# Kernel tuning notes

Measured on AMD Instinct MI355X. Metric: run time of the kernel, lower is better.

The kernel has to match this reference:

```python
import jax, jax.numpy as jnp
import numpy as np

B, S, RNN, ATT_HID = 64, 2048, 1024, 512


def setup_inputs() -> dict:
    key = jax.random.key(0)
    ks = jax.random.split(key, 8)
    h = jax.random.normal(ks[0], (B, RNN), dtype=jnp.float32)
    att_feats = jax.random.normal(ks[1], (B, S, RNN), dtype=jnp.float32)
    p_att_feats = jax.random.normal(ks[2], (B, S, ATT_HID), dtype=jnp.float32)
    att_masks = jax.random.randint(ks[3], (B, S), 0, 2, dtype=jnp.int32)
    # parameters of h2att: Linear(rnn_size -> att_hid_size)
    W_h = jax.random.normal(ks[4], (ATT_HID, RNN), dtype=jnp.float32) / np.sqrt(RNN)
    b_h = jnp.zeros((ATT_HID,), dtype=jnp.float32)
    # parameters of alpha_net: Linear(att_hid_size -> 1)
    w_a = jax.random.normal(ks[5], (ATT_HID,), dtype=jnp.float32) / np.sqrt(ATT_HID)
    b_a = jnp.zeros((), dtype=jnp.float32)
    return {"h": h, "att_feats": att_feats, "p_att_feats": p_att_feats,
            "att_masks": att_masks, "W_h": W_h, "b_h": b_h, "w_a": w_a, "b_a": b_a}


def reference(h, att_feats, p_att_feats, att_masks, W_h, b_h, w_a, b_a):
    # h: [B, rnn], p_att_feats: [B, S, att_hid], att_feats: [B, S, feat]
    att_h = h @ W_h.T + b_h                            # [B, att_hid]
    dot = jnp.tanh(p_att_feats + att_h[:, None, :])     # [B, S, att_hid]
    scores = jnp.einsum('bsh,h->bs', dot, w_a) + b_a    # [B, S]
    weight = jax.nn.softmax(scores, axis=1)             # [B, S]
    m = att_masks.astype(weight.dtype)
    weight = weight * m
    weight = weight / jnp.sum(weight, axis=1, keepdims=True)
    att_res = jnp.einsum('bs,bsd->bd', weight, att_feats)  # [B, feat]
    return att_res
```

## Files before the change

kernel.cpp:

```cpp
#include <hip/hip_runtime.h>

#define B_SZ 64
#define S_SZ 2048
#define RNN 1024
#define ATT 512
#define NCHUNK 32
#define CHUNK_S (S_SZ / NCHUNK)
#define KSPL 2

#define OFF_ATTHP  0
#define OFF_PART   65536
#define OFF_USUM   2162688

__device__ __forceinline__ float fast_tanh(float x) {
    float t = __builtin_exp2f(x * 2.885390082f);
    return 1.0f - 2.0f * __builtin_amdgcn_rcpf(t + 1.0f);
}

__global__ __launch_bounds__(128) void k_atth(const float* __restrict__ h,
                                              const float* __restrict__ Wh,
                                              float* __restrict__ att_h_part) {
    int b  = blockIdx.z;
    int ks = blockIdx.y;
    int j  = blockIdx.x * 128 + threadIdx.x;
    int kbase = ks * (RNN / KSPL);

    __shared__ float hs[RNN / KSPL];
    for (int i = threadIdx.x; i < RNN / KSPL; i += 128)
        hs[i] = h[(size_t)b * RNN + kbase + i];
    __syncthreads();

    const float4* w4 = (const float4*)(Wh + (size_t)j * RNN + kbase);
    const float4* h4 = (const float4*)hs;
    float a0 = 0.f, a1 = 0.f, a2 = 0.f, a3 = 0.f;
    #pragma unroll 4
    for (int k = 0; k < (RNN / KSPL) / 4; k += 4) {
        float4 w, hv;
        w = w4[k + 0]; hv = h4[k + 0];
        a0 += w.x * hv.x + w.y * hv.y + w.z * hv.z + w.w * hv.w;
        w = w4[k + 1]; hv = h4[k + 1];
        a1 += w.x * hv.x + w.y * hv.y + w.z * hv.z + w.w * hv.w;
        w = w4[k + 2]; hv = h4[k + 2];
        a2 += w.x * hv.x + w.y * hv.y + w.z * hv.z + w.w * hv.w;
        w = w4[k + 3]; hv = h4[k + 3];
        a3 += w.x * hv.x + w.y * hv.y + w.z * hv.z + w.w * hv.w;
    }
    att_h_part[((size_t)ks * B_SZ + b) * ATT + j] = (a0 + a1) + (a2 + a3);
}

__global__ __launch_bounds__(256) void k_fused(const float* __restrict__ p,
                                               const float* __restrict__ att_h_part,
                                               const float* __restrict__ bh,
                                               const float* __restrict__ w_a,
                                               const float* __restrict__ b_a,
                                               const int* __restrict__ mask,
                                               const float* __restrict__ feats,
                                               float* __restrict__ partials,
                                               float* __restrict__ usum) {
    int c = blockIdx.x;
    int b = blockIdx.y;
    int t = threadIdx.x;
    int s0 = c * CHUNK_S;

    __shared__ float ah[ATT];
    __shared__ float wa[ATT];
    __shared__ float u_c[CHUNK_S];
    __shared__ int   active[CHUNK_S];
    __shared__ int   nact_s;

    const float* ph0 = att_h_part + (size_t)b * ATT;
    const float* ph1 = att_h_part + ((size_t)B_SZ + b) * ATT;
    for (int i = t; i < ATT; i += 256) {
        ah[i] = ph0[i] + ph1[i] + bh[i];
        wa[i] = w_a[i];
    }
    if (t < CHUNK_S) {
        u_c[t] = 0.f;
        int m = mask[(size_t)b * S_SZ + s0 + t];
        unsigned long long bal = __ballot(m != 0);
        int rank = __popcll(bal & ((1ULL << (unsigned)t) - 1ULL));
        if (m) active[rank] = t;
        if (t == 0) nact_s = (int)__popcll(bal);
    }
    __syncthreads();
    int nact = nact_s;

    int wave = t >> 6;
    int lane = t & 63;
    float ba = b_a[0];

    const float4* ah4 = (const float4*)ah;
    const float4* wa4 = (const float4*)wa;
    float4 a0 = ah4[lane];
    float4 a1 = ah4[64 + lane];
    float4 w0 = wa4[lane];
    float4 w1 = wa4[64 + lane];

    const float4* pbase = (const float4*)(p + ((size_t)b * S_SZ + s0) * ATT);
    for (int k = wave; k < nact; k += 4) {
        int sl = active[k];
        const float4* p4 = pbase + (size_t)sl * 128;
        float4 x0 = p4[lane];
        float4 x1 = p4[64 + lane];

        float part;
        part  = w0.x * fast_tanh(x0.x + a0.x);
        part += w0.y * fast_tanh(x0.y + a0.y);
        part += w0.z * fast_tanh(x0.z + a0.z);
        part += w0.w * fast_tanh(x0.w + a0.w);
        part += w1.x * fast_tanh(x1.x + a1.x);
        part += w1.y * fast_tanh(x1.y + a1.y);
        part += w1.z * fast_tanh(x1.z + a1.z);
        part += w1.w * fast_tanh(x1.w + a1.w);

        #pragma unroll
        for (int off = 32; off > 0; off >>= 1)
            part += __shfl_xor(part, off, 64);

        if (lane == 0) {
            float sc = fminf(part + ba, 80.f);
            u_c[k] = __builtin_expf(sc);
        }
    }
    __syncthreads();

    const float4* f4 = (const float4*)(feats + ((size_t)b * S_SZ + s0) * RNN);
    float4 acc = {0.f, 0.f, 0.f, 0.f};
    int k = 0;
    for (; k + 4 <= nact; k += 4) {
        int r0 = active[k + 0], r1 = active[k + 1];
        int r2 = active[k + 2], r3 = active[k + 3];
        float g0 = u_c[k + 0], g1 = u_c[k + 1];
        float g2 = u_c[k + 2], g3 = u_c[k + 3];
        float4 v0 = f4[(size_t)r0 * 256 + t];
        float4 v1 = f4[(size_t)r1 * 256 + t];
        float4 v2 = f4[(size_t)r2 * 256 + t];
        float4 v3 = f4[(size_t)r3 * 256 + t];
        acc.x += g0 * v0.x; acc.y += g0 * v0.y; acc.z += g0 * v0.z; acc.w += g0 * v0.w;
        acc.x += g1 * v1.x; acc.y += g1 * v1.y; acc.z += g1 * v1.z; acc.w += g1 * v1.w;
        acc.x += g2 * v2.x; acc.y += g2 * v2.y; acc.z += g2 * v2.z; acc.w += g2 * v2.w;
        acc.x += g3 * v3.x; acc.y += g3 * v3.y; acc.z += g3 * v3.z; acc.w += g3 * v3.w;
    }
    for (; k < nact; ++k) {
        int r = active[k];
        float g = u_c[k];
        float4 v = f4[(size_t)r * 256 + t];
        acc.x += g * v.x; acc.y += g * v.y; acc.z += g * v.z; acc.w += g * v.w;
    }
    ((float4*)partials)[((size_t)b * NCHUNK + c) * 256 + t] = acc;

    if (wave == 0) {
        float s = u_c[lane];
        #pragma unroll
        for (int off = 32; off > 0; off >>= 1)
            s += __shfl_xor(s, off, 64);
        if (lane == 0) usum[(size_t)b * NCHUNK + c] = s;
    }
}

__global__ __launch_bounds__(256) void k_reduce(const float* __restrict__ partials,
                                                const float* __restrict__ usum,
                                                float* __restrict__ out) {
    int b = blockIdx.y;
    int j = blockIdx.x * 256 + threadIdx.x;

    float tot = 0.f;
    #pragma unroll
    for (int c = 0; c < NCHUNK; ++c)
        tot += usum[(size_t)b * NCHUNK + c];

    float acc = 0.f;
    #pragma unroll 8
    for (int c = 0; c < NCHUNK; ++c)
        acc += partials[((size_t)b * NCHUNK + c) * RNN + j];

    out[(size_t)b * RNN + j] = acc / tot;
}

extern "C" void kernel_launch(void* const* d_in, const int* in_sizes, int n_in,
                              void* d_out, int out_size, void* d_ws, size_t ws_size,
                              hipStream_t stream) {
    const float* h         = (const float*)d_in[0];
    const float* att_feats = (const float*)d_in[1];
    const float* p_att     = (const float*)d_in[2];
    const int*   att_masks = (const int*)d_in[3];
    const float* W_h       = (const float*)d_in[4];
    const float* b_h       = (const float*)d_in[5];
    const float* w_a       = (const float*)d_in[6];
    const float* b_a       = (const float*)d_in[7];
    float* out = (float*)d_out;

    float* wsf = (float*)d_ws;
    float* att_h_part = wsf + OFF_ATTHP;
    float* partials   = wsf + OFF_PART;
    float* usum       = wsf + OFF_USUM;

    k_atth<<<dim3(4, KSPL, B_SZ), 128, 0, stream>>>(h, W_h, att_h_part);
    k_fused<<<dim3(NCHUNK, B_SZ), 256, 0, stream>>>(p_att, att_h_part, b_h, w_a, b_a,
                                                    att_masks, att_feats,
                                                    partials, usum);
    k_reduce<<<dim3(RNN / 256, B_SZ), 256, 0, stream>>>(partials, usum, out);
}
```

Before: 103.7 us.

## Software-pipeline score computation with feature gather in 16-row tiles

```diff
diff --git a/kernel.cpp b/kernel.cpp
--- a/kernel.cpp
+++ b/kernel.cpp
@@ -48,15 +48,15 @@
     att_h_part[((size_t)ks * B_SZ + b) * ATT + j] = (a0 + a1) + (a2 + a3);
 }
 
-__global__ __launch_bounds__(256) void k_fused(const float* __restrict__ p,
-                                               const float* __restrict__ att_h_part,
-                                               const float* __restrict__ bh,
-                                               const float* __restrict__ w_a,
-                                               const float* __restrict__ b_a,
-                                               const int* __restrict__ mask,
-                                               const float* __restrict__ feats,
-                                               float* __restrict__ partials,
-                                               float* __restrict__ usum) {
+__global__ __launch_bounds__(256, 8) void k_fused(const float* __restrict__ p,
+                                                  const float* __restrict__ att_h_part,
+                                                  const float* __restrict__ bh,
+                                                  const float* __restrict__ w_a,
+                                                  const float* __restrict__ b_a,
+                                                  const int* __restrict__ mask,
+                                                  const float* __restrict__ feats,
+                                                  float* __restrict__ partials,
+                                                  float* __restrict__ usum) {
     int c = blockIdx.x;
     int b = blockIdx.y;
     int t = threadIdx.x;
@@ -64,8 +64,8 @@
 
     __shared__ float ah[ATT];
     __shared__ float wa[ATT];
-    __shared__ float u_c[CHUNK_S];
-    __shared__ int   active[CHUNK_S];
+    __shared__ __align__(16) float u_c[CHUNK_S];
+    __shared__ __align__(16) int   active[CHUNK_S];
     __shared__ int   nact_s;
 
     const float* ph0 = att_h_part + (size_t)b * ATT;
@@ -78,12 +78,19 @@
         u_c[t] = 0.f;
         int m = mask[(size_t)b * S_SZ + s0 + t];
         unsigned long long bal = __ballot(m != 0);
-        int rank = __popcll(bal & ((1ULL << (unsigned)t) - 1ULL));
-        if (m) active[rank] = t;
-        if (t == 0) nact_s = (int)__popcll(bal);
+        int na = (int)__popcll(bal);
+        unsigned long long below = (1ULL << (unsigned)t) - 1ULL;
+        if (m) {
+            active[__popcll(bal & below)] = t;
+        } else {
+            active[na + __popcll((~bal) & below)] = 0;
+        }
+        if (t == 0) nact_s = na;
     }
     __syncthreads();
     int nact = nact_s;
+    int n16 = (nact + 15) & ~15;
+    int n_tiles = n16 >> 4;
 
     int wave = t >> 6;
     int lane = t & 63;
@@ -97,56 +104,91 @@
     float4 w1 = wa4[64 + lane];
 
     const float4* pbase = (const float4*)(p + ((size_t)b * S_SZ + s0) * ATT);
-    for (int k = wave; k < nact; k += 4) {
-        int sl = active[k];
-        const float4* p4 = pbase + (size_t)sl * 128;
-        float4 x0 = p4[lane];
-        float4 x1 = p4[64 + lane];
-
-        float part;
-        part  = w0.x * fast_tanh(x0.x + a0.x);
-        part += w0.y * fast_tanh(x0.y + a0.y);
-        part += w0.z * fast_tanh(x0.z + a0.z);
-        part += w0.w * fast_tanh(x0.w + a0.w);
-        part += w1.x * fast_tanh(x1.x + a1.x);
-        part += w1.y * fast_tanh(x1.y + a1.y);
-        part += w1.z * fast_tanh(x1.z + a1.z);
-        part += w1.w * fast_tanh(x1.w + a1.w);
-
-        #pragma unroll
-        for (int off = 32; off > 0; off >>= 1)
-            part += __shfl_xor(part, off, 64);
-
-        if (lane == 0) {
-            float sc = fminf(part + ba, 80.f);
-            u_c[k] = __builtin_expf(sc);
+    const float4* f4 = (const float4*)(feats + ((size_t)b * S_SZ + s0) * RNN);
+    const int4*   act4 = (const int4*)active;
+    const float4* uc4  = (const float4*)u_c;
+    float4 acc = {0.f, 0.f, 0.f, 0.f};
+
+    #define SCORE_TILE(TILE)                                                    \
+    {                                                                           \
+        int base_ = ((TILE) << 4) + wave * 4;                                   \
+        _Pragma("unroll")                                                       \
+        for (int i_ = 0; i_ < 2; ++i_) {                                        \
+            int kA_ = base_ + i_ * 2, kB_ = kA_ + 1;                            \
+            int slA_ = active[kA_], slB_ = active[kB_];                         \
+            const float4* pA_ = pbase + (size_t)slA_ * 128;                     \
+            const float4* pB_ = pbase + (size_t)slB_ * 128;                     \
+            float4 xa0_ = pA_[lane];                                            \
+            float4 xa1_ = pA_[64 + lane];                                       \
+            float4 xb0_ = pB_[lane];                                            \
+            float4 xb1_ = pB_[64 + lane];                                       \
+            float pa_, pb_;                                                     \
+            pa_  = w0.x * fast_tanh(xa0_.x + a0.x);                             \
+            pa_ += w0.y * fast_tanh(xa0_.y + a0.y);                             \
+            pa_ += w0.z * fast_tanh(xa0_.z + a0.z);                             \
+            pa_ += w0.w * fast_tanh(xa0_.w + a0.w);                             \
+            pa_ += w1.x * fast_tanh(xa1_.x + a1.x);                             \
+            pa_ += w1.y * fast_tanh(xa1_.y + a1.y);                             \
+            pa_ += w1.z * fast_tanh(xa1_.z + a1.z);                             \
+            pa_ += w1.w * fast_tanh(xa1_.w + a1.w);                             \
+            pb_  = w0.x * fast_tanh(xb0_.x + a0.x);                             \
+            pb_ += w0.y * fast_tanh(xb0_.y + a0.y);                             \
+            pb_ += w0.z * fast_tanh(xb0_.z + a0.z);                             \
+            pb_ += w0.w * fast_tanh(xb0_.w + a0.w);                             \
+            pb_ += w1.x * fast_tanh(xb1_.x + a1.x);                             \
+            pb_ += w1.y * fast_tanh(xb1_.y + a1.y);                             \
+            pb_ += w1.z * fast_tanh(xb1_.z + a1.z);                             \
+            pb_ += w1.w * fast_tanh(xb1_.w + a1.w);                             \
+            _Pragma("unroll")                                                   \
+            for (int off_ = 32; off_ > 0; off_ >>= 1) {                         \
+                pa_ += __shfl_xor(pa_, off_, 64);                               \
+                pb_ += __shfl_xor(pb_, off_, 64);                               \
+            }                                                                   \
+            if (lane == 0) {                                                    \
+                if (kA_ < nact) u_c[kA_] = __builtin_expf(fminf(pa_ + ba, 80.f)); \
+                if (kB_ < nact) u_c[kB_] = __builtin_expf(fminf(pb_ + ba, 80.f)); \
+            }                                                                   \
+        }                                                                       \
+    }
+
+    #define GATHER_TILE(TILE)                                                   \
+    {                                                                           \
+        _Pragma("unroll")                                                       \
+        for (int kk_ = 0; kk_ < 2; ++kk_) {                                     \
+            int q_ = ((TILE) << 2) + kk_ * 2;                                   \
+            int4  r0_ = act4[q_];                                               \
+            int4  r1_ = act4[q_ + 1];                                           \
+            float4 g0_ = uc4[q_];                                               \
+            float4 g1_ = uc4[q_ + 1];                                           \
+            float4 v0_ = f4[(size_t)r0_.x * 256 + t];                           \
+            float4 v1_ = f4[(size_t)r0_.y * 256 + t];                           \
+            float4 v2_ = f4[(size_t)r0_.z * 256 + t];                           \
+            float4 v3_ = f4[(size_t)r0_.w * 256 + t];                           \
+            float4 v4_ = f4[(size_t)r1_.x * 256 + t];                           \
+            float4 v5_ = f4[(size_t)r1_.y * 256 + t];                           \
+            float4 v6_ = f4[(size_t)r1_.z * 256 + t];                           \
+            float4 v7_ = f4[(size_t)r1_.w * 256 + t];                           \
+            acc.x += g0_.x * v0_.x; acc.y += g0_.x * v0_.y; acc.z += g0_.x * v0_.z; acc.w += g0_.x * v0_.w; \
+            acc.x += g0_.y * v1_.x; acc.y += g0_.y * v1_.y; acc.z += g0_.y * v1_.z; acc.w += g0_.y * v1_.w; \
+            acc.x += g0_.z * v2_.x; acc.y += g0_.z * v2_.y; acc.z += g0_.z * v2_.z; acc.w += g0_.z * v2_.w; \
+            acc.x += g0_.w * v3_.x; acc.y += g0_.w * v3_.y; acc.z += g0_.w * v3_.z; acc.w += g0_.w * v3_.w; \
+            acc.x += g1_.x * v4_.x; acc.y += g1_.x * v4_.y; acc.z += g1_.x * v4_.z; acc.w += g1_.x * v4_.w; \
+            acc.x += g1_.y * v5_.x; acc.y += g1_.y * v5_.y; acc.z += g1_.y * v5_.z; acc.w += g1_.y * v5_.w; \
+            acc.x += g1_.z * v6_.x; acc.y += g1_.z * v6_.y; acc.z += g1_.z * v6_.z; acc.w += g1_.z * v6_.w; \
+            acc.x += g1_.w * v7_.x; acc.y += g1_.w * v7_.y; acc.z += g1_.w * v7_.z; acc.w += g1_.w * v7_.w; \
+        }                                                                       \
+    }
+
+    if (n_tiles > 0) {
+        SCORE_TILE(0);
+        __syncthreads();
+        for (int st = 0; st < n_tiles; ++st) {
+            if (st + 1 < n_tiles) SCORE_TILE(st + 1);
+            GATHER_TILE(st);
+            __syncthreads();
         }
     }
-    __syncthreads();
-
-    const float4* f4 = (const float4*)(feats + ((size_t)b * S_SZ + s0) * RNN);
-    float4 acc = {0.f, 0.f, 0.f, 0.f};
-    int k = 0;
-    for (; k + 4 <= nact; k += 4) {
-        int r0 = active[k + 0], r1 = active[k + 1];
-        int r2 = active[k + 2], r3 = active[k + 3];
-        float g0 = u_c[k + 0], g1 = u_c[k + 1];
-        float g2 = u_c[k + 2], g3 = u_c[k + 3];
-        float4 v0 = f4[(size_t)r0 * 256 + t];
-        float4 v1 = f4[(size_t)r1 * 256 + t];
-        float4 v2 = f4[(size_t)r2 * 256 + t];
-        float4 v3 = f4[(size_t)r3 * 256 + t];
-        acc.x += g0 * v0.x; acc.y += g0 * v0.y; acc.z += g0 * v0.z; acc.w += g0 * v0.w;
-        acc.x += g1 * v1.x; acc.y += g1 * v1.y; acc.z += g1 * v1.z; acc.w += g1 * v1.w;
-        acc.x += g2 * v2.x; acc.y += g2 * v2.y; acc.z += g2 * v2.z; acc.w += g2 * v2.w;
-        acc.x += g3 * v3.x; acc.y += g3 * v3.y; acc.z += g3 * v3.z; acc.w += g3 * v3.w;
-    }
-    for (; k < nact; ++k) {
-        int r = active[k];
-        float g = u_c[k];
-        float4 v = f4[(size_t)r * 256 + t];
-        acc.x += g * v.x; acc.y += g * v.y; acc.z += g * v.z; acc.w += g * v.w;
-    }
+
     ((float4*)partials)[((size_t)b * NCHUNK + c) * 256 + t] = acc;
 
     if (wave == 0) {
```

Result: slower. 134.6 us (+29.8%).

## Split score and gather phases, gather over column slices with compacted row list

Applied to the files above, without the earlier changes.

```diff
diff --git a/kernel.cpp b/kernel.cpp
--- a/kernel.cpp
+++ b/kernel.cpp
@@ -5,12 +5,11 @@
 #define RNN 1024
 #define ATT 512
 #define NCHUNK 32
-#define CHUNK_S (S_SZ / NCHUNK)
+#define CHUNK_S 64
 #define KSPL 2
 
-#define OFF_ATTHP  0
-#define OFF_PART   65536
-#define OFF_USUM   2162688
+#define OFF_ATTHP 0
+#define OFF_U     65536
 
 __device__ __forceinline__ float fast_tanh(float x) {
     float t = __builtin_exp2f(x * 2.885390082f);
@@ -48,15 +47,13 @@
     att_h_part[((size_t)ks * B_SZ + b) * ATT + j] = (a0 + a1) + (a2 + a3);
 }
 
-__global__ __launch_bounds__(256) void k_fused(const float* __restrict__ p,
-                                               const float* __restrict__ att_h_part,
-                                               const float* __restrict__ bh,
-                                               const float* __restrict__ w_a,
-                                               const float* __restrict__ b_a,
-                                               const int* __restrict__ mask,
-                                               const float* __restrict__ feats,
-                                               float* __restrict__ partials,
-                                               float* __restrict__ usum) {
+__global__ __launch_bounds__(256, 8) void k_scores(const float* __restrict__ p,
+                                                   const float* __restrict__ att_h_part,
+                                                   const float* __restrict__ bh,
+                                                   const float* __restrict__ w_a,
+                                                   const float* __restrict__ b_a,
+                                                   const int* __restrict__ mask,
+                                                   float* __restrict__ u_g) {
     int c = blockIdx.x;
     int b = blockIdx.y;
     int t = threadIdx.x;
@@ -64,7 +61,7 @@
 
     __shared__ float ah[ATT];
     __shared__ float wa[ATT];
-    __shared__ float u_c[CHUNK_S];
+    __shared__ float u_d[CHUNK_S];
     __shared__ int   active[CHUNK_S];
     __shared__ int   nact_s;
 
@@ -75,7 +72,7 @@
         wa[i] = w_a[i];
     }
     if (t < CHUNK_S) {
-        u_c[t] = 0.f;
+        u_d[t] = 0.f;
         int m = mask[(size_t)b * S_SZ + s0 + t];
         unsigned long long bal = __ballot(m != 0);
         int rank = __popcll(bal & ((1ULL << (unsigned)t) - 1ULL));
@@ -117,64 +114,119 @@
         for (int off = 32; off > 0; off >>= 1)
             part += __shfl_xor(part, off, 64);
 
-        if (lane == 0) {
-            float sc = fminf(part + ba, 80.f);
-            u_c[k] = __builtin_expf(sc);
+        if (lane == 0)
+            u_d[sl] = __builtin_expf(fminf(part + ba, 80.f));
+    }
+    __syncthreads();
+
+    if (t < CHUNK_S)
+        u_g[(size_t)b * S_SZ + s0 + t] = u_d[t];
+}
+
+__global__ __launch_bounds__(512, 2) void k_gather(const float* __restrict__ feats,
+                                                   const float* __restrict__ u_g,
+                                                   float* __restrict__ out) {
+    int js = blockIdx.x;
+    int b  = blockIdx.y;
+    int t  = threadIdx.x;
+    int wave = t >> 6, lane = t & 63;
+
+    __shared__ __align__(16) float          cw[2112];
+    __shared__ __align__(16) unsigned short crow[2112];
+    __shared__ int   counts[32];
+    __shared__ int   offs[32];
+    __shared__ float wsum[8];
+    __shared__ __align__(16) float red[8 * 256];
+    __shared__ int   ntot_s, n64_s;
+    __shared__ float inv_s;
+
+    float u_r[4];
+    unsigned long long bal_r[4];
+    float psum = 0.f;
+    #pragma unroll
+    for (int r = 0; r < 4; ++r) {
+        int chunk = wave * 4 + r;
+        u_r[r] = u_g[(size_t)b * S_SZ + chunk * 64 + lane];
+        psum += u_r[r];
+        bal_r[r] = __ballot(u_r[r] > 0.f);
+        if (lane == 0) counts[chunk] = (int)__popcll(bal_r[r]);
+    }
+    #pragma unroll
+    for (int off = 32; off > 0; off >>= 1)
+        psum += __shfl_xor(psum, off, 64);
+    if (lane == 0) wsum[wave] = psum;
+    __syncthreads();
+
+    if (t == 0) {
+        int o = 0;
+        #pragma unroll
+        for (int c2 = 0; c2 < 32; ++c2) { offs[c2] = o; o += counts[c2]; }
+        ntot_s = o;
+        n64_s = (o + 63) & ~63;
+        float us = ((wsum[0] + wsum[1]) + (wsum[2] + wsum[3]))
+                 + ((wsum[4] + wsum[5]) + (wsum[6] + wsum[7]));
+        inv_s = 1.f / us;
+    }
+    __syncthreads();
+    int ntot = ntot_s, n64 = n64_s;
+
+    for (int k = ntot + t; k < n64; k += 512) { crow[k] = 0; cw[k] = 0.f; }
+    #pragma unroll
+    for (int r = 0; r < 4; ++r) {
+        int chunk = wave * 4 + r;
+        if (u_r[r] > 0.f) {
+            int rank = (int)__popcll(bal_r[r] & ((1ULL << (unsigned)lane) - 1ULL));
+            int pos = offs[chunk] + rank;
+            crow[pos] = (unsigned short)(chunk * 64 + lane);
+            cw[pos]   = u_r[r];
         }
     }
     __syncthreads();
 
-    const float4* f4 = (const float4*)(feats + ((size_t)b * S_SZ + s0) * RNN);
+    const float4* fb = (const float4*)(feats + (size_t)b * S_SZ * RNN);
+    int colb = js * 64 + lane;
+    const uint4*  crow4 = (const uint4*)crow;
+    const float4* cw4   = (const float4*)cw;
     float4 acc = {0.f, 0.f, 0.f, 0.f};
-    int k = 0;
-    for (; k + 4 <= nact; k += 4) {
-        int r0 = active[k + 0], r1 = active[k + 1];
-        int r2 = active[k + 2], r3 = active[k + 3];
-        float g0 = u_c[k + 0], g1 = u_c[k + 1];
-        float g2 = u_c[k + 2], g3 = u_c[k + 3];
-        float4 v0 = f4[(size_t)r0 * 256 + t];
-        float4 v1 = f4[(size_t)r1 * 256 + t];
-        float4 v2 = f4[(size_t)r2 * 256 + t];
-        float4 v3 = f4[(size_t)r3 * 256 + t];
-        acc.x += g0 * v0.x; acc.y += g0 * v0.y; acc.z += g0 * v0.z; acc.w += g0 * v0.w;
-        acc.x += g1 * v1.x; acc.y += g1 * v1.y; acc.z += g1 * v1.z; acc.w += g1 * v1.w;
-        acc.x += g2 * v2.x; acc.y += g2 * v2.y; acc.z += g2 * v2.z; acc.w += g2 * v2.w;
-        acc.x += g3 * v3.x; acc.y += g3 * v3.y; acc.z += g3 * v3.z; acc.w += g3 * v3.w;
-    }
-    for (; k < nact; ++k) {
-        int r = active[k];
-        float g = u_c[k];
-        float4 v = f4[(size_t)r * 256 + t];
-        acc.x += g * v.x; acc.y += g * v.y; acc.z += g * v.z; acc.w += g * v.w;
-    }
-    ((float4*)partials)[((size_t)b * NCHUNK + c) * 256 + t] = acc;
+    for (int k0 = wave * 8; k0 < n64; k0 += 64) {
+        uint4  rr = crow4[k0 >> 3];
+        float4 ga = cw4[k0 >> 2];
+        float4 gb = cw4[(k0 >> 2) + 1];
+        int r0 = rr.x & 0xFFFF, r1 = (int)(rr.x >> 16);
+        int r2 = rr.y & 0xFFFF, r3 = (int)(rr.y >> 16);
+        int r4 = rr.z & 0xFFFF, r5 = (int)(rr.z >> 16);
+        int r6 = rr.w & 0xFFFF, r7 = (int)(rr.w >> 16);
+        float4 v0 = fb[(size_t)r0 * 256 + colb];
+        float4 v1 = fb[(size_t)r1 * 256 + colb];
+        float4 v2 = fb[(size_t)r2 * 256 + colb];
+        float4 v3 = fb[(size_t)r3 * 256 + colb];
+        float4 v4 = fb[(size_t)r4 * 256 + colb];
+        float4 v5 = fb[(size_t)r5 * 256 + colb];
+        float4 v6 = fb[(size_t)r6 * 256 + colb];
+        float4 v7 = fb[(size_t)r7 * 256 + colb];
+        acc.x += ga.x * v0.x; acc.y += ga.x * v0.y; acc.z += ga.x * v0.z; acc.w += ga.x * v0.w;
+        acc.x += ga.y * v1.x; acc.y += ga.y * v1.y; acc.z += ga.y * v1.z; acc.w += ga.y * v1.w;
+        acc.x += ga.z * v2.x; acc.y += ga.z * v2.y; acc.z += ga.z * v2.z; acc.w += ga.z * v2.w;
+        acc.x += ga.w * v3.x; acc.y += ga.w * v3.y; acc.z += ga.w * v3.z; acc.w += ga.w * v3.w;
+        acc.x += gb.x * v4.x; acc.y += gb.x * v4.y; acc.z += gb.x * v4.z; acc.w += gb.x * v4.w;
+        acc.x += gb.y * v5.x; acc.y += gb.y * v5.y; acc.z += gb.y * v5.z; acc.w += gb.y * v5.w;
+        acc.x += gb.z * v6.x; acc.y += gb.z * v6.y; acc.z += gb.z * v6.z; acc.w += gb.z * v6.w;
+        acc.x += gb.w * v7.x; acc.y += gb.w * v7.y; acc.z += gb.w * v7.z; acc.w += gb.w * v7.w;
+    }
+    ((float4*)red)[wave * 64 + lane] = acc;
+    __syncthreads();
 
     if (wave == 0) {
-        float s = u_c[lane];
+        float4 s = {0.f, 0.f, 0.f, 0.f};
         #pragma unroll
-        for (int off = 32; off > 0; off >>= 1)
-            s += __shfl_xor(s, off, 64);
-        if (lane == 0) usum[(size_t)b * NCHUNK + c] = s;
-    }
-}
-
-__global__ __launch_bounds__(256) void k_reduce(const float* __restrict__ partials,
-                                                const float* __restrict__ usum,
-                                                float* __restrict__ out) {
-    int b = blockIdx.y;
-    int j = blockIdx.x * 256 + threadIdx.x;
-
-    float tot = 0.f;
-    #pragma unroll
-    for (int c = 0; c < NCHUNK; ++c)
-        tot += usum[(size_t)b * NCHUNK + c];
-
-    float acc = 0.f;
-    #pragma unroll 8
-    for (int c = 0; c < NCHUNK; ++c)
-        acc += partials[((size_t)b * NCHUNK + c) * RNN + j];
-
-    out[(size_t)b * RNN + j] = acc / tot;
+        for (int w2 = 0; w2 < 8; ++w2) {
+            float4 v = ((const float4*)red)[w2 * 64 + lane];
+            s.x += v.x; s.y += v.y; s.z += v.z; s.w += v.w;
+        }
+        float inv = inv_s;
+        float4 o4 = {s.x * inv, s.y * inv, s.z * inv, s.w * inv};
+        ((float4*)out)[(size_t)b * 256 + js * 64 + lane] = o4;
+    }
 }
 
 extern "C" void kernel_launch(void* const* d_in, const int* in_sizes, int n_in,
@@ -192,12 +244,10 @@
 
     float* wsf = (float*)d_ws;
     float* att_h_part = wsf + OFF_ATTHP;
-    float* partials   = wsf + OFF_PART;
-    float* usum       = wsf + OFF_USUM;
+    float* u_g        = wsf + OFF_U;
 
     k_atth<<<dim3(4, KSPL, B_SZ), 128, 0, stream>>>(h, W_h, att_h_part);
-    k_fused<<<dim3(NCHUNK, B_SZ), 256, 0, stream>>>(p_att, att_h_part, b_h, w_a, b_a,
-                                                    att_masks, att_feats,
-                                                    partials, usum);
-    k_reduce<<<dim3(RNN / 256, B_SZ), 256, 0, stream>>>(partials, usum, out);
-}
+    k_scores<<<dim3(NCHUNK, B_SZ), 256, 0, stream>>>(p_att, att_h_part, b_h, w_a, b_a,
+                                                     att_masks, u_g);
+    k_gather<<<dim3(4, B_SZ), 512, 0, stream>>>(att_feats, u_g, out);
+}
```

Measured after the change: 99.92 us. -3.7%, faster.
